# Kernel optimization log

Measured on AMD Instinct MI355X. Metric: run time of the kernel, lower is better.

## Reference

```python
import jax, jax.numpy as jnp
import numpy as np

B, L, D, H, NL, S = 256, 256, 4, 1024, 2, 100
OUT = D - 1  # noise_start_seq_z is sliced [:, :, :-1]


def setup_inputs() -> dict:
    key = jax.random.key(0)
    ks = jax.random.split(key, 32)
    f32 = jnp.float32
    p = lambda i, shape, s=0.05: (s * jax.random.normal(ks[i], shape)).astype(f32)
    alphas = (1.0 - 0.02 * jax.random.uniform(ks[3], (S,))).astype(f32)  # DDPM-style schedule
    inp = {
        "batch_size": B, "seq_len": L, "dim_seq": D, "num_diffusion_steps": S,
        "noise_start_seq_z": jax.random.normal(ks[0], (B, L, D), f32),
        "initial_noise": 0.3 * jax.random.normal(ks[1], (B, D), f32),  # noise_scale=0.3 (BM=False)
        "step_noise": jax.random.normal(ks[2], (S, B, 1, 1), f32),
        "alphas": alphas,
        "betas": 1.0 - alphas,
        "baralphas": jnp.cumprod(alphas),
        # initial_nn (for h0) and initial_nn1 (for c0): residual MLP D -> H -> H -> NL*H
        "A1a": p(4, (H, D)), "b1a": p(5, (H,)), "A2a": p(6, (H, H)), "b2a": p(7, (H,)),
        "A3a": p(8, (NL * H, H)), "b3a": p(9, (NL * H,)),
        "A1b": p(10, (H, D)), "b1b": p(11, (H,)), "A2b": p(12, (H, H)), "b2b": p(13, (H,)),
        "A3b": p(14, (NL * H, H)), "b3b": p(15, (NL * H,)),
        # 2-layer LSTM, PyTorch layout: W_ih [4H, in], W_hh [4H, H], gate order i,f,g,o
        "Wih0": p(16, (4 * H, OUT * L)), "Whh0": p(17, (4 * H, H)),
        "bih0": p(18, (4 * H,)), "bhh0": p(19, (4 * H,)),
        "Wih1": p(20, (4 * H, H)), "Whh1": p(21, (4 * H, H)),
        "bih1": p(22, (4 * H,)), "bhh1": p(23, (4 * H,)),
        "Wlin": p(24, (OUT * L, H)),  # Linear, bias=False
    }
    return inp


def _resnet(x, A1, b1, A2, b2, A3, b3):
    h1 = jax.nn.relu(x @ A1.T + b1)
    h2 = jax.nn.relu(h1 @ A2.T + b2) + h1  # residual on matching dims
    return jnp.tanh(h2 @ A3.T + b3)        # nn.Tanh() wrapper


def _cell(x, h, c, Wih, Whh, bih, bhh):
    g = x @ Wih.T + bih + h @ Whh.T + bhh
    i, f, gg, o = jnp.split(g, 4, axis=-1)
    c2 = jax.nn.sigmoid(f) * c + jax.nn.sigmoid(i) * jnp.tanh(gg)
    return jax.nn.sigmoid(o) * jnp.tanh(c2), c2


def _forward(z, n0, sn, alphas, betas, baralphas,
             A1a, b1a, A2a, b2a, A3a, b3a, A1b, b1b, A2b, b2b, A3b, b3b,
             Wih0, Whh0, bih0, bhh0, Wih1, Whh1, bih1, bhh1, Wlin):
    Bz, Lz, Dz = z.shape
    out_dim = Dz - 1
    steps = alphas.shape[0]
    Hh = Whh0.shape[1]
    prev0 = z[:, :, :-1]                               # (B, L, out_dim)
    hn = _resnet(n0, A1a, b1a, A2a, b2a, A3a, b3a).reshape(Bz, -1, Hh).transpose(1, 0, 2)
    cn = _resnet(n0, A1b, b1b, A2b, b2b, A3b, b3b).reshape(Bz, -1, Hh).transpose(1, 0, 2)

    def step(carry, xs):
        h, c, prev = carry
        i, noise = xs
        idx = steps - i
        x = prev.reshape(Bz, Lz * out_dim)
        h0n, c0n = _cell(x, h[0], c[0], Wih0, Whh0, bih0, bhh0)
        h1n, c1n = _cell(h0n, h[1], c[1], Wih1, Whh1, bih1, bhh1)
        dec = (jnp.tanh(h1n) @ Wlin.T).reshape(Bz, Lz, out_dim)
        a, ba, be = alphas[idx], baralphas[idx], betas[idx]
        dec = (prev - (1.0 - a) / jnp.sqrt(1.0 - ba) * dec) / jnp.sqrt(a)
        dec = dec + jnp.where(i + 1 < steps, jnp.sqrt(be) * noise, jnp.float32(0.0))
        return (jnp.stack([h0n, h1n]), jnp.stack([c0n, c1n]), dec), dec

    xs = (jnp.arange(1, steps), sn[1:])
    _, ys = jax.lax.scan(step, (hn, cn, prev0), xs)
    outputs = jnp.concatenate([prev0[None], ys], axis=0)  # (steps, B, L, out_dim)
    return outputs[::-1]                                  # flip(0)


def reference(batch_size, seq_len, dim_seq, num_diffusion_steps,
              noise_start_seq_z, initial_noise, step_noise, alphas, betas, baralphas,
              A1a, b1a, A2a, b2a, A3a, b3a, A1b, b1b, A2b, b2b, A3b, b3b,
              Wih0, Whh0, bih0, bhh0, Wih1, Whh1, bih1, bhh1, Wlin):
    assert noise_start_seq_z.shape == (batch_size, seq_len, dim_seq)
    assert alphas.shape[0] == num_diffusion_steps
    return _forward(noise_start_seq_z, initial_noise, step_noise, alphas, betas, baralphas,
                    A1a, b1a, A2a, b2a, A3a, b3a, A1b, b1b, A2b, b2b, A3b, b3b,
                    Wih0, Whh0, bih0, bhh0, Wih1, Whh1, bih1, bhh1, Wlin)
```

## Files before the change

### kernel.cpp

```cpp
#include <hip/hip_runtime.h>
#include <hip/hip_bf16.h>
#include <math.h>

#define BB 256
#define LL 256
#define DD 4
#define HH 1024
#define SS 100
#define OUTD 3
#define X0 768
#define K1 1792
#define K2 2048
#define NG 4096
#define BKB 128

typedef __attribute__((ext_vector_type(4))) float f32x4;
typedef __attribute__((ext_vector_type(8))) short bf16x8;
typedef __hip_bfloat16 bf16;

__device__ __forceinline__ float sigmoidf_(float x){ return 1.0f/(1.0f + __expf(-x)); }

__device__ __forceinline__ void gll16(const void* g, void* l){
  __builtin_amdgcn_global_load_lds((const __attribute__((address_space(1))) unsigned int*)g,
                                   (__attribute__((address_space(3))) unsigned int*)l, 16, 0, 0);
}

template<int K, bool WTANH>
__global__ __launch_bounds__(512) void cell_v2(
    const bf16* __restrict__ Acat, const bf16* __restrict__ Wcat,
    const float* __restrict__ bias, float* __restrict__ cst,
    bf16* __restrict__ dstA, int ldA, bf16* __restrict__ dstB, int ldB)
{
  __shared__ __align__(16) char smem[49152];
  const int tid  = threadIdx.x;
  const int wave = tid >> 6, lane = tid & 63;
  const int m0 = blockIdx.x * 64;
  const int n0 = blockIdx.y * 32;
  const int wm = wave >> 2, wn = wave & 3;
  const int l7 = lane & 7, l3 = lane >> 3;
  const int swz = 16 * (l7 ^ l3);

  const char* src[3];
  char* dstL[2][3];
  #pragma unroll
  for (int i = 0; i < 3; i++){
    int c = wave*3 + i;
    const bf16* base; size_t roff; int ldsoff;
    if (c < 8){
      int row = c*8 + l3;
      base = Acat; roff = (size_t)(m0 + row) * K; ldsoff = c*1024;
    } else {
      int wr = (c-8)*8 + l3;
      int g = wr >> 5, j = wr & 31;
      base = Wcat; roff = (size_t)(g*HH + n0 + j) * K; ldsoff = 8192 + (c-8)*1024;
    }
    src[i] = (const char*)(base + roff) + swz;
    dstL[0][i] = smem + ldsoff;
    dstL[1][i] = smem + 24576 + ldsoff;
  }

  const int lr = lane & 15, kq = lane >> 4;
  const int rsw = (lr & 7) << 4;
  int offA[2][2], offB[2][2];
  #pragma unroll
  for (int mt = 0; mt < 2; mt++)
    #pragma unroll
    for (int s = 0; s < 2; s++){
      int row = wm*32 + mt*16 + lr;
      offA[mt][s] = row*BKB + ((s*64 + kq*16) ^ rsw);
    }
  #pragma unroll
  for (int nt = 0; nt < 2; nt++)
    #pragma unroll
    for (int s = 0; s < 2; s++){
      int wr = wn*32 + nt*16 + lr;
      offB[nt][s] = 8192 + wr*BKB + ((s*64 + kq*16) ^ rsw);
    }

  f32x4 acc[2][2] = {};
  constexpr int NT = K / 64;

  #pragma unroll
  for (int i = 0; i < 3; i++) gll16(src[i], dstL[0][i]);

  for (int t = 0; t < NT; ++t){
    const int b = t & 1;
    if (t + 1 < NT){
      #pragma unroll
      for (int i = 0; i < 3; i++) gll16(src[i] + (size_t)(t+1)*BKB, dstL[(t+1)&1][i]);
      asm volatile("s_waitcnt vmcnt(3)" ::: "memory");
    } else {
      asm volatile("s_waitcnt vmcnt(0)" ::: "memory");
    }
    __builtin_amdgcn_s_barrier();
    __builtin_amdgcn_sched_barrier(0);

    const char* cbase = smem + b*24576;
    bf16x8 Af[2][2], Bf[2][2];
    #pragma unroll
    for (int mt = 0; mt < 2; mt++)
      #pragma unroll
      for (int s = 0; s < 2; s++) Af[mt][s] = *(const bf16x8*)(cbase + offA[mt][s]);
    #pragma unroll
    for (int nt = 0; nt < 2; nt++)
      #pragma unroll
      for (int s = 0; s < 2; s++) Bf[nt][s] = *(const bf16x8*)(cbase + offB[nt][s]);
    #pragma unroll
    for (int s = 0; s < 2; s++)
      #pragma unroll
      for (int mt = 0; mt < 2; mt++)
        #pragma unroll
        for (int nt = 0; nt < 2; nt++)
          acc[mt][nt] = __builtin_amdgcn_mfma_f32_16x16x32_bf16(Af[mt][s], Bf[nt][s], acc[mt][nt], 0,0,0);

    __builtin_amdgcn_sched_barrier(0);
    __builtin_amdgcn_s_barrier();
  }

  float* g_lds = (float*)smem;
  const int cr = lane & 15, rq = lane >> 4;
  #pragma unroll
  for (int mt = 0; mt < 2; mt++)
    #pragma unroll
    for (int nt = 0; nt < 2; nt++)
      #pragma unroll
      for (int j = 0; j < 4; j++){
        int r = mt*16 + rq*4 + j;
        int cc = nt*16 + cr;
        g_lds[((wm*4 + wn)*32 + r)*32 + cc] = acc[mt][nt][j];
      }
  __syncthreads();
  #pragma unroll
  for (int e = 0; e < 4; e++){
    int idx = tid + e*512;
    int ml = idx >> 5, nl = idx & 31;
    int w2 = ml >> 5, r = ml & 31;
    int m = m0 + ml, n = n0 + nl;
    float gi = g_lds[((w2*4+0)*32 + r)*32 + nl] + bias[n];
    float gf = g_lds[((w2*4+1)*32 + r)*32 + nl] + bias[HH + n];
    float gg = g_lds[((w2*4+2)*32 + r)*32 + nl] + bias[2*HH + n];
    float go = g_lds[((w2*4+3)*32 + r)*32 + nl] + bias[3*HH + n];
    float cold = cst[m*HH + n];
    float cn = sigmoidf_(gf)*cold + sigmoidf_(gi)*tanhf(gg);
    float hn = sigmoidf_(go)*tanhf(cn);
    cst[m*HH + n] = cn;
    dstA[(size_t)m*ldA + n] = __float2bfloat16(hn);
    dstB[(size_t)m*ldB + n] = __float2bfloat16(WTANH ? tanhf(hn) : hn);
  }
}

__global__ __launch_bounds__(512) void dec_v2(
    const bf16* __restrict__ th, const bf16* __restrict__ Wl,
    const float* __restrict__ alphas, const float* __restrict__ betas,
    const float* __restrict__ baralphas, const float* __restrict__ snoise,
    float* __restrict__ prev, float* __restrict__ out,
    bf16* __restrict__ xnext, int t)
{
  __shared__ __align__(16) char smem[32768];
  const int tid  = threadIdx.x;
  const int wave = tid >> 6, lane = tid & 63;
  const int m0 = blockIdx.x * 64;
  const int n0 = blockIdx.y * 64;
  const int wm = wave >> 2, wn = wave & 3;
  const int l7 = lane & 7, l3 = lane >> 3;
  const int swz = 16 * (l7 ^ l3);

  const char* src[2];
  char* dstL[2][2];
  #pragma unroll
  for (int i = 0; i < 2; i++){
    int c = wave*2 + i;
    const bf16* base; size_t roff; int ldsoff;
    if (c < 8){ int row = c*8 + l3; base = th; roff = (size_t)(m0 + row)*HH; ldsoff = c*1024; }
    else { int wr = (c-8)*8 + l3;  base = Wl; roff = (size_t)(n0 + wr)*HH; ldsoff = 8192 + (c-8)*1024; }
    src[i] = (const char*)(base + roff) + swz;
    dstL[0][i] = smem + ldsoff;
    dstL[1][i] = smem + 16384 + ldsoff;
  }

  const int lr = lane & 15, kq = lane >> 4;
  const int rsw = (lr & 7) << 4;
  int offA[2][2], offB[2];
  #pragma unroll
  for (int mt = 0; mt < 2; mt++)
    #pragma unroll
    for (int s = 0; s < 2; s++){
      int row = wm*32 + mt*16 + lr;
      offA[mt][s] = row*BKB + ((s*64 + kq*16) ^ rsw);
    }
  #pragma unroll
  for (int s = 0; s < 2; s++){
    int wr = wn*16 + lr;
    offB[s] = 8192 + wr*BKB + ((s*64 + kq*16) ^ rsw);
  }

  f32x4 acc[2] = {};
  constexpr int NT = HH / 64;
  #pragma unroll
  for (int i = 0; i < 2; i++) gll16(src[i], dstL[0][i]);

  for (int tt = 0; tt < NT; ++tt){
    const int b = tt & 1;
    if (tt + 1 < NT){
      #pragma unroll
      for (int i = 0; i < 2; i++) gll16(src[i] + (size_t)(tt+1)*BKB, dstL[(tt+1)&1][i]);
      asm volatile("s_waitcnt vmcnt(2)" ::: "memory");
    } else {
      asm volatile("s_waitcnt vmcnt(0)" ::: "memory");
    }
    __builtin_amdgcn_s_barrier();
    __builtin_amdgcn_sched_barrier(0);

    const char* cbase = smem + b*16384;
    bf16x8 Af[2][2], Bf[2];
    #pragma unroll
    for (int mt = 0; mt < 2; mt++)
      #pragma unroll
      for (int s = 0; s < 2; s++) Af[mt][s] = *(const bf16x8*)(cbase + offA[mt][s]);
    #pragma unroll
    for (int s = 0; s < 2; s++) Bf[s] = *(const bf16x8*)(cbase + offB[s]);
    #pragma unroll
    for (int s = 0; s < 2; s++)
      #pragma unroll
      for (int mt = 0; mt < 2; mt++)
        acc[mt] = __builtin_amdgcn_mfma_f32_16x16x32_bf16(Af[mt][s], Bf[s], acc[mt], 0,0,0);

    __builtin_amdgcn_sched_barrier(0);
    __builtin_amdgcn_s_barrier();
  }

  const int idxs = SS - t;
  float a = alphas[idxs], ba = baralphas[idxs], be = betas[idxs];
  float coef = (1.0f - a) / sqrtf(1.0f - ba);
  float isq  = 1.0f / sqrtf(a);
  float nf = (t+1 < SS) ? sqrtf(be) : 0.0f;
  float* outp = out + (size_t)(SS-1-t) * (BB*X0);
  const int cr = lane & 15, rq = lane >> 4;
  #pragma unroll
  for (int mt = 0; mt < 2; mt++)
    #pragma unroll
    for (int j = 0; j < 4; j++){
      int m = m0 + wm*32 + mt*16 + rq*4 + j;
      int n = n0 + wn*16 + cr;
      float d = acc[mt][j];
      float p = prev[m*X0 + n];
      float dec = (p - coef*d)*isq + nf*snoise[t*BB + m];
      outp[m*X0 + n] = dec;
      prev[m*X0 + n] = dec;
      xnext[(size_t)m*K1 + n] = __float2bfloat16(dec);
    }
}

__device__ __forceinline__ void gemm32x32(const bf16* __restrict__ A, int lda,
                                          const bf16* __restrict__ W, int ldw,
                                          int m0, int wr0, int K,
                                          f32x4 acc[2][2], int lane)
{
  int r  = lane & 15;
  int kq = lane >> 4;
  const bf16* a0 = A + (size_t)(m0 + r)      * lda + kq*8;
  const bf16* a1 = A + (size_t)(m0 + 16 + r) * lda + kq*8;
  const bf16* b0 = W + (size_t)(wr0 + r)      * ldw + kq*8;
  const bf16* b1 = W + (size_t)(wr0 + 16 + r) * ldw + kq*8;
  for (int kk = 0; kk < K; kk += 32) {
    bf16x8 av0 = *(const bf16x8*)(a0 + kk);
    bf16x8 av1 = *(const bf16x8*)(a1 + kk);
    bf16x8 bv0 = *(const bf16x8*)(b0 + kk);
    bf16x8 bv1 = *(const bf16x8*)(b1 + kk);
    acc[0][0] = __builtin_amdgcn_mfma_f32_16x16x32_bf16(av0, bv0, acc[0][0], 0,0,0);
    acc[0][1] = __builtin_amdgcn_mfma_f32_16x16x32_bf16(av0, bv1, acc[0][1], 0,0,0);
    acc[1][0] = __builtin_amdgcn_mfma_f32_16x16x32_bf16(av1, bv0, acc[1][0], 0,0,0);
    acc[1][1] = __builtin_amdgcn_mfma_f32_16x16x32_bf16(av1, bv1, acc[1][1], 0,0,0);
  }
}

template<int EPI>
__global__ __launch_bounds__(256) void rgemm_kernel(
    const bf16* __restrict__ A, const bf16* __restrict__ W,
    const float* __restrict__ bias, const float* __restrict__ resid,
    bf16* __restrict__ d1, int ld1, bf16* __restrict__ d2, int ld2,
    float* __restrict__ f1, float* __restrict__ f2)
{
  int tid=threadIdx.x, wave=tid>>6, lane=tid&63;
  int m0 = blockIdx.x*32;
  int n0 = (blockIdx.y*4+wave)*32;
  f32x4 acc[2][2] = {};
  gemm32x32(A, HH, W, HH, m0, n0, HH, acc, lane);
  int cr=lane&15, rq=lane>>4;
  for (int r=0;r<2;r++) for (int c=0;c<2;c++) for (int j=0;j<4;j++) {
    int m = m0 + r*16+rq*4+j, n = n0 + c*16+cr;
    float v = acc[r][c][j] + bias[n];
    if (EPI==0) {
      float h = fmaxf(v,0.f) + resid[m*HH+n];
      d1[(size_t)m*ld1+n] = __float2bfloat16(h);
    } else if (EPI==1) {
      float tv = tanhf(v);
      if (n < HH) d1[(size_t)m*ld1+n] = __float2bfloat16(tv);
      else        d2[(size_t)m*ld2 + (n-HH)] = __float2bfloat16(tv);
    } else {
      float tv = tanhf(v);
      if (n < HH) f1[m*HH+n] = tv;
      else        f2[m*HH + (n-HH)] = tv;
    }
  }
}

__global__ void prep_w0_kernel(const float* __restrict__ Wih0, const float* __restrict__ Whh0,
                               bf16* __restrict__ W0cat){
  int i = blockIdx.x*256 + threadIdx.x;
  if (i >= NG*K1) return;
  int n = i / K1, k = i % K1;
  float v = (k < X0) ? Wih0[n*X0 + k] : Whh0[n*HH + (k - X0)];
  W0cat[i] = __float2bfloat16(v);
}
__global__ void prep_w1_kernel(const float* __restrict__ Wih1, const float* __restrict__ Whh1,
                               bf16* __restrict__ W1cat){
  int i = blockIdx.x*256 + threadIdx.x;
  if (i >= NG*K2) return;
  int n = i / K2, k = i % K2;
  float v = (k < HH) ? Wih1[n*HH + k] : Whh1[n*HH + (k - HH)];
  W1cat[i] = __float2bfloat16(v);
}
__global__ void cvt_kernel(const float* __restrict__ s, bf16* __restrict__ d, int n){
  int i = blockIdx.x*256 + threadIdx.x;
  if (i < n) d[i] = __float2bfloat16(s[i]);
}
__global__ void prep_bias_kernel(const float* bih0, const float* bhh0,
                                 const float* bih1, const float* bhh1,
                                 float* b0, float* b1){
  int i = blockIdx.x*256 + threadIdx.x;
  if (i < NG){ b0[i] = bih0[i] + bhh0[i]; b1[i] = bih1[i] + bhh1[i]; }
}
__global__ void init_x_kernel(const float* __restrict__ z, float* __restrict__ prev,
                              bf16* __restrict__ xcat1, float* __restrict__ out){
  int i = blockIdx.x*256 + threadIdx.x;
  if (i >= BB*X0) return;
  int m = i / X0, col = i % X0;
  int l = col / OUTD, d = col % OUTD;
  float v = z[(size_t)(m*LL + l)*DD + d];
  prev[i] = v;
  out[(size_t)(SS-1)*BB*X0 + i] = v;
  xcat1[(size_t)m*K1 + col] = __float2bfloat16(v);
}
__global__ void r1_kernel(const float* __restrict__ n0,
    const float* __restrict__ A1a, const float* __restrict__ b1a,
    const float* __restrict__ A1b, const float* __restrict__ b1b,
    float* __restrict__ h1fa, bf16* __restrict__ h1ba,
    float* __restrict__ h1fb, bf16* __restrict__ h1bb){
  int gid = blockIdx.x*256 + threadIdx.x;
  if (gid >= BB*2*HH) return;
  int m = gid >> 11;
  int col = gid & 2047;
  const float* A1; const float* b1; float* hf; bf16* hb; int c;
  if (col < HH){ A1=A1a; b1=b1a; hf=h1fa; hb=h1ba; c=col; }
  else         { A1=A1b; b1=b1b; hf=h1fb; hb=h1bb; c=col-HH; }
  float v = b1[c];
  for (int d=0; d<DD; d++) v += n0[m*DD + d] * A1[c*DD + d];
  v = fmaxf(v, 0.f);
  hf[m*HH + c] = v;
  hb[m*HH + c] = __float2bfloat16(v);
}

static inline size_t alup(size_t x){ return (x + 255) & ~(size_t)255; }

extern "C" void kernel_launch(void* const* d_in, const int* in_sizes, int n_in,
                              void* d_out, int out_size, void* d_ws, size_t ws_size,
                              hipStream_t stream) {
  const float* z      = (const float*)d_in[4];
  const float* n0     = (const float*)d_in[5];
  const float* snoise = (const float*)d_in[6];
  const float* alphas = (const float*)d_in[7];
  const float* betas  = (const float*)d_in[8];
  const float* barals = (const float*)d_in[9];
  const float* A1a = (const float*)d_in[10]; const float* b1a = (const float*)d_in[11];
  const float* A2a = (const float*)d_in[12]; const float* b2a = (const float*)d_in[13];
  const float* A3a = (const float*)d_in[14]; const float* b3a = (const float*)d_in[15];
  const float* A1b = (const float*)d_in[16]; const float* b1b = (const float*)d_in[17];
  const float* A2b = (const float*)d_in[18]; const float* b2b = (const float*)d_in[19];
  const float* A3b = (const float*)d_in[20]; const float* b3b = (const float*)d_in[21];
  const float* Wih0 = (const float*)d_in[22]; const float* Whh0 = (const float*)d_in[23];
  const float* bih0 = (const float*)d_in[24]; const float* bhh0 = (const float*)d_in[25];
  const float* Wih1 = (const float*)d_in[26]; const float* Whh1 = (const float*)d_in[27];
  const float* bih1 = (const float*)d_in[28]; const float* bhh1 = (const float*)d_in[29];
  const float* Wlin = (const float*)d_in[30];
  float* out = (float*)d_out;

  char* p = (char*)d_ws;
  size_t off = 0;
  auto take = [&](size_t bytes)->char*{ char* r = p + off; off = alup(off + bytes); return r; };
  bf16* W0cat = (bf16*)take((size_t)NG*K1*2);
  bf16* W1cat = (bf16*)take((size_t)NG*K2*2);
  bf16* WlinB = (bf16*)take((size_t)X0*HH*2);
  bf16* A2aB  = (bf16*)take((size_t)HH*HH*2);
  bf16* A2bB  = (bf16*)take((size_t)HH*HH*2);
  bf16* A3aB  = (bf16*)take((size_t)2*HH*HH*2);
  bf16* A3bB  = (bf16*)take((size_t)2*HH*HH*2);
  float* bias0 = (float*)take(NG*4);
  float* bias1 = (float*)take(NG*4);
  bf16* xcat0 = (bf16*)take((size_t)BB*K1*2);
  bf16* xcat1 = (bf16*)take((size_t)BB*K1*2);
  bf16* x2_0  = (bf16*)take((size_t)BB*K2*2);
  bf16* x2_1  = (bf16*)take((size_t)BB*K2*2);
  bf16* th    = (bf16*)take((size_t)BB*HH*2);
  float* c0   = (float*)take((size_t)BB*HH*4);
  float* c1   = (float*)take((size_t)BB*HH*4);
  float* prev = (float*)take((size_t)BB*X0*4);
  float* h1fa = (float*)take((size_t)BB*HH*4);
  float* h1fb = (float*)take((size_t)BB*HH*4);
  bf16* h1ba  = (bf16*)take((size_t)BB*HH*2);
  bf16* h1bb  = (bf16*)take((size_t)BB*HH*2);
  bf16* h2ba  = (bf16*)take((size_t)BB*HH*2);
  bf16* h2bb  = (bf16*)take((size_t)BB*HH*2);
  (void)ws_size; (void)in_sizes; (void)n_in; (void)out_size;

  prep_w0_kernel<<<(NG*K1+255)/256, 256, 0, stream>>>(Wih0, Whh0, W0cat);
  prep_w1_kernel<<<(NG*K2+255)/256, 256, 0, stream>>>(Wih1, Whh1, W1cat);
  cvt_kernel<<<(X0*HH+255)/256, 256, 0, stream>>>(Wlin, WlinB, X0*HH);
  cvt_kernel<<<(HH*HH+255)/256, 256, 0, stream>>>(A2a, A2aB, HH*HH);
  cvt_kernel<<<(HH*HH+255)/256, 256, 0, stream>>>(A2b, A2bB, HH*HH);
  cvt_kernel<<<(2*HH*HH+255)/256, 256, 0, stream>>>(A3a, A3aB, 2*HH*HH);
  cvt_kernel<<<(2*HH*HH+255)/256, 256, 0, stream>>>(A3b, A3bB, 2*HH*HH);
  prep_bias_kernel<<<(NG+255)/256, 256, 0, stream>>>(bih0, bhh0, bih1, bhh1, bias0, bias1);
  init_x_kernel<<<(BB*X0+255)/256, 256, 0, stream>>>(z, prev, xcat1, out);
  r1_kernel<<<(BB*2*HH+255)/256, 256, 0, stream>>>(n0, A1a, b1a, A1b, b1b, h1fa, h1ba, h1fb, h1bb);
  rgemm_kernel<0><<<dim3(8,8), 256, 0, stream>>>(h1ba, A2aB, b2a, h1fa, h2ba, HH, nullptr, 0, nullptr, nullptr);
  rgemm_kernel<0><<<dim3(8,8), 256, 0, stream>>>(h1bb, A2bB, b2b, h1fb, h2bb, HH, nullptr, 0, nullptr, nullptr);
  rgemm_kernel<1><<<dim3(8,16), 256, 0, stream>>>(h2ba, A3aB, b3a, nullptr, xcat1 + X0, K1, x2_1 + HH, K2, nullptr, nullptr);
  rgemm_kernel<2><<<dim3(8,16), 256, 0, stream>>>(h2bb, A3bB, b3b, nullptr, nullptr, 0, nullptr, 0, c0, c1);

  for (int t = 1; t < SS; t++) {
    bf16* xc  = (t & 1) ? xcat1 : xcat0;
    bf16* xn  = (t & 1) ? xcat0 : xcat1;
    bf16* x2c = (t & 1) ? x2_1 : x2_0;
    bf16* x2n = (t & 1) ? x2_0 : x2_1;
    cell_v2<K1,false><<<dim3(4,32), 512, 0, stream>>>(
        xc, W0cat, bias0, c0, x2c, K2, xn + X0, K1);
    cell_v2<K2,true><<<dim3(4,32), 512, 0, stream>>>(
        x2c, W1cat, bias1, c1, x2n + HH, K2, th, HH);
    dec_v2<<<dim3(4,12), 512, 0, stream>>>(
        th, WlinB, alphas, betas, barals, snoise, prev, out, xn, t);
  }
}
```

Before: 4.049 ms.

## Restructure LSTM cell GEMM with split-K waves, gate-interleaved weights, XCD-aware tiling

Replaces the LSTM cell kernel with a 256-thread variant. Each block computes a 64x64 tile of gate-interleaved outputs, and two wave pairs split K in half and reduce through LDS. The weight rows are reordered at prep time so the four gates of a hidden unit sit next to each other, which allows vectorized epilogue reads. Blocks are mapped so that N-tiles sharing weights land on the same XCD. The A operand is loaded straight from global memory into registers with double buffering, and only the weights are staged through LDS. The aim is better weight reuse and locality in L2 and per XCD, and less LDS traffic for A, at the cost of lower occupancy, a split-K reduction step and a larger LDS footprint.

```diff
diff --git a/kernel.cpp b/kernel.cpp
--- a/kernel.cpp
+++ b/kernel.cpp
@@ -25,127 +25,159 @@
                                    (__attribute__((address_space(3))) unsigned int*)l, 16, 0, 0);
 }
 
-template<int K, bool WTANH>
-__global__ __launch_bounds__(512) void cell_v2(
-    const bf16* __restrict__ Acat, const bf16* __restrict__ Wcat,
-    const float* __restrict__ bias, float* __restrict__ cst,
+template<int K, int KH, bool WTANH>
+__global__ __launch_bounds__(256, 1) void cell_v4(
+    const bf16* __restrict__ Acat,
+    const bf16* __restrict__ Wr,
+    const float* __restrict__ biasr,
+    float* __restrict__ cst,
     bf16* __restrict__ dstA, int ldA, bf16* __restrict__ dstB, int ldB)
 {
-  __shared__ __align__(16) char smem[49152];
+  constexpr int NT = KH / 128;
+  __shared__ __align__(16) char smem[81920];
+
   const int tid  = threadIdx.x;
   const int wave = tid >> 6, lane = tid & 63;
-  const int m0 = blockIdx.x * 64;
-  const int n0 = blockIdx.y * 32;
-  const int wm = wave >> 2, wn = wave & 3;
-  const int l7 = lane & 7, l3 = lane >> 3;
-  const int swz = 16 * (l7 ^ l3);
-
-  const char* src[3];
-  char* dstL[2][3];
-  #pragma unroll
-  for (int i = 0; i < 3; i++){
-    int c = wave*3 + i;
-    const bf16* base; size_t roff; int ldsoff;
-    if (c < 8){
-      int row = c*8 + l3;
-      base = Acat; roff = (size_t)(m0 + row) * K; ldsoff = c*1024;
-    } else {
-      int wr = (c-8)*8 + l3;
-      int g = wr >> 5, j = wr & 31;
-      base = Wcat; roff = (size_t)(g*HH + n0 + j) * K; ldsoff = 8192 + (c-8)*1024;
-    }
-    src[i] = (const char*)(base + roff) + swz;
-    dstL[0][i] = smem + ldsoff;
-    dstL[1][i] = smem + 24576 + ldsoff;
-  }
-
-  const int lr = lane & 15, kq = lane >> 4;
-  const int rsw = (lr & 7) << 4;
-  int offA[2][2], offB[2][2];
+  const int wm = wave & 1, wk = wave >> 1;
+  const int lr = lane & 15, kq16 = lane >> 4;
+
+  const int bid = blockIdx.x;
+  const int xcd = bid & 7, within = bid >> 3;
+  const int ntile = xcd * 8 + (within & 7);
+  const int mtile = within >> 3;
+  const int m0 = mtile * 64;
+  const int n0 = ntile * 64;
+
+  const char* srcW[8];
+  int ldsoff[8];
+  #pragma unroll
+  for (int j = 0; j < 8; j++){
+    int c = wm*8 + j;
+    int row = c*4 + (lane >> 4);
+    int slot = (lane & 15) ^ (row & 7);
+    srcW[j] = (const char*)(Wr + (size_t)(n0 + row) * K + wk * KH) + slot * 16;
+    ldsoff[j] = c * 1024;
+  }
+
+  const char* aptr[2];
   #pragma unroll
   for (int mt = 0; mt < 2; mt++)
-    #pragma unroll
-    for (int s = 0; s < 2; s++){
-      int row = wm*32 + mt*16 + lr;
-      offA[mt][s] = row*BKB + ((s*64 + kq*16) ^ rsw);
-    }
-  #pragma unroll
-  for (int nt = 0; nt < 2; nt++)
-    #pragma unroll
-    for (int s = 0; s < 2; s++){
-      int wr = wn*32 + nt*16 + lr;
-      offB[nt][s] = 8192 + wr*BKB + ((s*64 + kq*16) ^ rsw);
-    }
-
-  f32x4 acc[2][2] = {};
-  constexpr int NT = K / 64;
-
-  #pragma unroll
-  for (int i = 0; i < 3; i++) gll16(src[i], dstL[0][i]);
-
-  for (int t = 0; t < NT; ++t){
-    const int b = t & 1;
-    if (t + 1 < NT){
-      #pragma unroll
-      for (int i = 0; i < 3; i++) gll16(src[i] + (size_t)(t+1)*BKB, dstL[(t+1)&1][i]);
-      asm volatile("s_waitcnt vmcnt(3)" ::: "memory");
-    } else {
-      asm volatile("s_waitcnt vmcnt(0)" ::: "memory");
-    }
-    __builtin_amdgcn_s_barrier();
+    aptr[mt] = (const char*)(Acat + (size_t)(m0 + wm*32 + mt*16 + lr) * K + wk * KH) + kq16 * 16;
+
+  int woff[4][4];
+  #pragma unroll
+  for (int nt = 0; nt < 4; nt++)
+    #pragma unroll
+    for (int s = 0; s < 4; s++){
+      int row = nt*16 + lr;
+      woff[nt][s] = row*256 + (((s*4 + kq16) ^ (row & 7)) << 4);
+    }
+
+  f32x4 acc[2][4] = {};
+  bf16x8 Aa[2][4], Ab[2][4];
+
+  {
+    char* db = smem + wk*32768;
+    #pragma unroll
+    for (int j = 0; j < 8; j++) gll16(srcW[j], db + ldsoff[j]);
     __builtin_amdgcn_sched_barrier(0);
-
-    const char* cbase = smem + b*24576;
-    bf16x8 Af[2][2], Bf[2][2];
     #pragma unroll
     for (int mt = 0; mt < 2; mt++)
       #pragma unroll
-      for (int s = 0; s < 2; s++) Af[mt][s] = *(const bf16x8*)(cbase + offA[mt][s]);
-    #pragma unroll
-    for (int nt = 0; nt < 2; nt++)
-      #pragma unroll
-      for (int s = 0; s < 2; s++) Bf[nt][s] = *(const bf16x8*)(cbase + offB[nt][s]);
-    #pragma unroll
-    for (int s = 0; s < 2; s++)
-      #pragma unroll
-      for (int mt = 0; mt < 2; mt++)
+      for (int s = 0; s < 4; s++)
+        Aa[mt][s] = *(const bf16x8*)(aptr[mt] + s*64);
+  }
+
+#define CELL_BODY(I, CUR, NXT, LAST)                                          \
+  {                                                                           \
+    __builtin_amdgcn_s_barrier();                                             \
+    if (!(LAST)) {                                                            \
+      char* db = smem + wk*32768 + (((I)+1)&1)*16384;                         \
+      _Pragma("unroll")                                                       \
+      for (int j = 0; j < 8; j++)                                             \
+        gll16(srcW[j] + (size_t)((I)+1)*256, db + ldsoff[j]);                 \
+      __builtin_amdgcn_sched_barrier(0);                                      \
+      _Pragma("unroll")                                                       \
+      for (int mt = 0; mt < 2; mt++)                                          \
+        _Pragma("unroll")                                                     \
+        for (int s = 0; s < 4; s++)                                           \
+          NXT[mt][s] = *(const bf16x8*)(aptr[mt] + (size_t)((I)+1)*256 + s*64);\
+      asm volatile("s_waitcnt vmcnt(16)" ::: "memory");                       \
+    } else {                                                                  \
+      asm volatile("s_waitcnt vmcnt(0)" ::: "memory");                        \
+    }                                                                         \
+    __builtin_amdgcn_s_barrier();                                             \
+    __builtin_amdgcn_sched_barrier(0);                                        \
+    const char* wb = smem + wk*32768 + ((I)&1)*16384;                         \
+    bf16x8 Wf[4][4];                                                          \
+    _Pragma("unroll")                                                         \
+    for (int nt = 0; nt < 4; nt++)                                            \
+      _Pragma("unroll")                                                       \
+      for (int s = 0; s < 4; s++)                                             \
+        Wf[nt][s] = *(const bf16x8*)(wb + woff[nt][s]);                       \
+    _Pragma("unroll")                                                         \
+    for (int s = 0; s < 4; s++)                                               \
+      _Pragma("unroll")                                                       \
+      for (int mt = 0; mt < 2; mt++)                                          \
+        _Pragma("unroll")                                                     \
+        for (int nt = 0; nt < 4; nt++)                                        \
+          acc[mt][nt] = __builtin_amdgcn_mfma_f32_16x16x32_bf16(              \
+              CUR[mt][s], Wf[nt][s], acc[mt][nt], 0,0,0);                     \
+    __builtin_amdgcn_sched_barrier(0);                                        \
+  }
+
+  {
+    int i = 0;
+    for (; i + 2 <= NT; i += 2){
+      CELL_BODY(i,   Aa, Ab, false);
+      CELL_BODY(i+1, Ab, Aa, ((i+2==NT) && !(NT & 1)));
+    }
+    if (NT & 1) CELL_BODY(NT-1, Aa, Ab, true);
+  }
+#undef CELL_BODY
+
+  float* gbuf = (float*)(smem + 65536);
+  const int rq = lane >> 4, cr = lane & 15;
+  __syncthreads();
+  if (wk == 0){
+    #pragma unroll
+    for (int mt = 0; mt < 2; mt++)
+      #pragma unroll
+      for (int nt = 0; nt < 4; nt++)
         #pragma unroll
-        for (int nt = 0; nt < 2; nt++)
-          acc[mt][nt] = __builtin_amdgcn_mfma_f32_16x16x32_bf16(Af[mt][s], Bf[nt][s], acc[mt][nt], 0,0,0);
-
-    __builtin_amdgcn_sched_barrier(0);
-    __builtin_amdgcn_s_barrier();
-  }
-
-  float* g_lds = (float*)smem;
-  const int cr = lane & 15, rq = lane >> 4;
-  #pragma unroll
-  for (int mt = 0; mt < 2; mt++)
-    #pragma unroll
-    for (int nt = 0; nt < 2; nt++)
-      #pragma unroll
-      for (int j = 0; j < 4; j++){
-        int r = mt*16 + rq*4 + j;
-        int cc = nt*16 + cr;
-        g_lds[((wm*4 + wn)*32 + r)*32 + cc] = acc[mt][nt][j];
-      }
+        for (int j = 0; j < 4; j++)
+          gbuf[(wm*32 + mt*16 + rq*4 + j)*64 + nt*16 + cr] = acc[mt][nt][j];
+  }
   __syncthreads();
+  if (wk == 1){
+    #pragma unroll
+    for (int mt = 0; mt < 2; mt++)
+      #pragma unroll
+      for (int nt = 0; nt < 4; nt++)
+        #pragma unroll
+        for (int j = 0; j < 4; j++)
+          gbuf[(wm*32 + mt*16 + rq*4 + j)*64 + nt*16 + cr] += acc[mt][nt][j];
+  }
+  __syncthreads();
+
   #pragma unroll
   for (int e = 0; e < 4; e++){
-    int idx = tid + e*512;
-    int ml = idx >> 5, nl = idx & 31;
-    int w2 = ml >> 5, r = ml & 31;
-    int m = m0 + ml, n = n0 + nl;
-    float gi = g_lds[((w2*4+0)*32 + r)*32 + nl] + bias[n];
-    float gf = g_lds[((w2*4+1)*32 + r)*32 + nl] + bias[HH + n];
-    float gg = g_lds[((w2*4+2)*32 + r)*32 + nl] + bias[2*HH + n];
-    float go = g_lds[((w2*4+3)*32 + r)*32 + nl] + bias[3*HH + n];
-    float cold = cst[m*HH + n];
+    int idx = e*256 + tid;
+    int r = idx >> 4, cl = idx & 15;
+    f32x4 g  = *(const f32x4*)&gbuf[r*64 + cl*4];
+    f32x4 bi = *(const f32x4*)&biasr[n0 + cl*4];
+    int m = m0 + r;
+    int col = ntile*16 + cl;
+    float gi = g[0] + bi[0];
+    float gf = g[1] + bi[1];
+    float gg = g[2] + bi[2];
+    float go = g[3] + bi[3];
+    float cold = cst[m*HH + col];
     float cn = sigmoidf_(gf)*cold + sigmoidf_(gi)*tanhf(gg);
     float hn = sigmoidf_(go)*tanhf(cn);
-    cst[m*HH + n] = cn;
-    dstA[(size_t)m*ldA + n] = __float2bfloat16(hn);
-    dstB[(size_t)m*ldB + n] = __float2bfloat16(WTANH ? tanhf(hn) : hn);
+    cst[m*HH + col] = cn;
+    dstA[(size_t)m*ldA + col] = __float2bfloat16(hn);
+    dstB[(size_t)m*ldB + col] = __float2bfloat16(WTANH ? tanhf(hn) : hn);
   }
 }
 
@@ -306,20 +338,24 @@
 }
 
 __global__ void prep_w0_kernel(const float* __restrict__ Wih0, const float* __restrict__ Whh0,
-                               bf16* __restrict__ W0cat){
+                               bf16* __restrict__ W0r){
   int i = blockIdx.x*256 + threadIdx.x;
   if (i >= NG*K1) return;
-  int n = i / K1, k = i % K1;
-  float v = (k < X0) ? Wih0[n*X0 + k] : Whh0[n*HH + (k - X0)];
-  W0cat[i] = __float2bfloat16(v);
+  int np = i / K1, k = i % K1;
+  int col = np >> 2, g = np & 3;
+  int srow = g*HH + col;
+  float v = (k < X0) ? Wih0[srow*X0 + k] : Whh0[srow*HH + (k - X0)];
+  W0r[i] = __float2bfloat16(v);
 }
 __global__ void prep_w1_kernel(const float* __restrict__ Wih1, const float* __restrict__ Whh1,
-                               bf16* __restrict__ W1cat){
+                               bf16* __restrict__ W1r){
   int i = blockIdx.x*256 + threadIdx.x;
   if (i >= NG*K2) return;
-  int n = i / K2, k = i % K2;
-  float v = (k < HH) ? Wih1[n*HH + k] : Whh1[n*HH + (k - HH)];
-  W1cat[i] = __float2bfloat16(v);
+  int np = i / K2, k = i % K2;
+  int col = np >> 2, g = np & 3;
+  int srow = g*HH + col;
+  float v = (k < HH) ? Wih1[srow*HH + k] : Whh1[srow*HH + (k - HH)];
+  W1r[i] = __float2bfloat16(v);
 }
 __global__ void cvt_kernel(const float* __restrict__ s, bf16* __restrict__ d, int n){
   int i = blockIdx.x*256 + threadIdx.x;
@@ -329,7 +365,12 @@
                                  const float* bih1, const float* bhh1,
                                  float* b0, float* b1){
   int i = blockIdx.x*256 + threadIdx.x;
-  if (i < NG){ b0[i] = bih0[i] + bhh0[i]; b1[i] = bih1[i] + bhh1[i]; }
+  if (i < NG){
+    int col = i >> 2, g = i & 3;
+    int s = g*HH + col;
+    b0[i] = bih0[s] + bhh0[s];
+    b1[i] = bih1[s] + bhh1[s];
+  }
 }
 __global__ void init_x_kernel(const float* __restrict__ z, float* __restrict__ prev,
                               bf16* __restrict__ xcat1, float* __restrict__ out){
@@ -433,9 +474,9 @@
     bf16* xn  = (t & 1) ? xcat0 : xcat1;
     bf16* x2c = (t & 1) ? x2_1 : x2_0;
     bf16* x2n = (t & 1) ? x2_0 : x2_1;
-    cell_v2<K1,false><<<dim3(4,32), 512, 0, stream>>>(
+    cell_v4<K1, 896, false><<<256, 256, 0, stream>>>(
         xc, W0cat, bias0, c0, x2c, K2, xn + X0, K1);
-    cell_v2<K2,true><<<dim3(4,32), 512, 0, stream>>>(
+    cell_v4<K2, 1024, true><<<256, 256, 0, stream>>>(
         x2c, W1cat, bias1, c1, x2n + HH, K2, th, HH);
     dec_v2<<<dim3(4,12), 512, 0, stream>>>(
         th, WlinB, alphas, betas, barals, snoise, prev, out, xn, t);
```

Result: no change. 4.071 ms (+0.6%).
